# Kernel optimization log

Measured on AMD Instinct MI355X. Metric: run time of the kernel, lower is better.

Reference implementation:

```python
import jax, jax.numpy as jnp
import numpy as np

DIM = 512
NUM_HEADS = 8
HEAD_DIM = DIM // NUM_HEADS
LOCAL_HEADS = 4
WINDOW = 64
NEG_INF = -1e9


def setup_inputs() -> dict:
    key = jax.random.key(0)
    ks = jax.random.split(key, 5)
    B, N, C = 4, 8192, DIM
    x = jax.random.normal(ks[0], (B, N, C), dtype=jnp.float32)
    # nn.Linear weights stored as [out, in]; xavier-ish scale
    s = (2.0 / (C + C)) ** 0.5
    Wq = jax.random.normal(ks[1], (C, C), dtype=jnp.float32) * s
    Wkv = jax.random.normal(ks[2], (C, C), dtype=jnp.float32) * s
    Wproj = jax.random.normal(ks[3], (C, C), dtype=jnp.float32) * s
    bproj = jax.random.normal(ks[4], (C,), dtype=jnp.float32) * 0.01
    return {"x": x, "Wq": Wq, "Wkv": Wkv, "Wproj": Wproj, "bproj": bproj}


def _look_around(t):
    # t: [B,H,nw,m,d] -> [B,H,nw,3m,d] (prev window, current, next; zero-padded at ends)
    p = jnp.pad(t, ((0, 0), (0, 0), (1, 1), (0, 0), (0, 0)))
    return jnp.concatenate([p[:, :, :-2], p[:, :, 1:-1], p[:, :, 2:]], axis=3)


def _local_attn(q, k, v, m):
    # non-causal LocalAttention, look_backward=1, look_forward=1
    B, H, N, d = q.shape
    nw = N // m
    scale = d ** -0.5
    qw = q.reshape(B, H, nw, m, d)
    kw = _look_around(k.reshape(B, H, nw, m, d))
    vw = _look_around(v.reshape(B, H, nw, m, d))
    # mask out look-around positions that fall outside the sequence
    pos = jnp.arange(N).reshape(nw, m)
    pp = jnp.pad(pos, ((1, 1), (0, 0)), constant_values=-1)
    kpos = jnp.concatenate([pp[:-2], pp[1:-1], pp[2:]], axis=1)  # [nw, 3m]
    valid = (kpos >= 0)[None, None, :, None, :]
    scores = jnp.einsum('bhwid,bhwjd->bhwij', qw * scale, kw)
    scores = jnp.where(valid, scores, NEG_INF)
    attn = jax.nn.softmax(scores, axis=-1)
    out = jnp.einsum('bhwij,bhwjd->bhwid', attn, vw)
    return out.reshape(B, H, N, d)


def _linear_attn(q, k, v):
    d = q.shape[-1]
    q = jax.nn.softmax(q, axis=-1) * (d ** -0.5)
    k = jax.nn.softmax(k, axis=-2)
    context = jnp.einsum('bhnd,bhne->bhde', k, v)
    return jnp.einsum('bhnd,bhde->bhne', q, context)


def reference(x, Wq, Wkv, Wproj, bproj):
    B, N, C = x.shape
    m = WINDOW
    original_N = N
    rem = N % m  # static; 0 for chosen shapes
    if rem > 0:
        x = jnp.pad(x, ((0, 0), (m - rem, 0), (0, 0)))
        N = x.shape[1]
    q = x @ Wq.T
    k = x @ Wkv.T
    v = x @ Wkv.T  # source uses the same kv linear for both k and v
    merge = lambda t: t.reshape(B, N, -1, HEAD_DIM).transpose(0, 2, 1, 3)  # [B,H,N,d]
    q, k, v = merge(q), merge(k), merge(v)
    lh = LOCAL_HEADS
    lq, gq = q[:, :lh], q[:, lh:]
    lk, gk = k[:, :lh], k[:, lh:]
    lv, gv = v[:, :lh], v[:, lh:]
    outs = []
    if lh > 0:
        outs.append(_local_attn(lq, lk, lv, m))
    if q.shape[1] - lh > 0:
        outs.append(_linear_attn(gq, gk, gv))
    attn = jnp.concatenate(outs, axis=1)  # [B,H,N,d]
    y = attn.transpose(0, 2, 1, 3).reshape(B, N, -1)
    y = y[:, -original_N:]
    y = y @ Wproj.T + bproj
    return (y, attn)
```

## Files before the change

kernel.cpp:

```cpp
#include <hip/hip_runtime.h>

#define DIM 512
#define NH 8
#define HD 64
#define LH 4
#define WIN 64
#define BATCH 4
#define SEQ 8192
#define NWIN (SEQ/WIN)

typedef unsigned short u16;
typedef __bf16 bf16x8 __attribute__((ext_vector_type(8)));
typedef float f32x4 __attribute__((ext_vector_type(4)));

__device__ __forceinline__ float b2f(u16 u) {
    return __uint_as_float(((unsigned int)u) << 16);
}
__device__ __forceinline__ u16 f2b(float f) {
    unsigned int x = __float_as_uint(f);
    return (u16)((x + 0x7FFFu + ((x >> 16) & 1u)) >> 16);
}

__device__ __forceinline__ void gload16(const void* g, void* l) {
    __builtin_amdgcn_global_load_lds(
        (__attribute__((address_space(1))) void*)g,
        (__attribute__((address_space(3))) void*)l, 16, 0, 0);
}

__global__ void convert_bf16(const float* __restrict__ src, u16* __restrict__ dst, long n)
{
    long i = ((long)blockIdx.x * 256 + threadIdx.x) * 8;
    const long stride = (long)gridDim.x * 256 * 8;
    for (; i < n; i += stride) {
        uint4 a = *(const uint4*)(src + i), b = *(const uint4*)(src + i + 4);
        const float* af = (const float*)&a;
        const float* bf_ = (const float*)&b;
        uint4 o; u16* ou = (u16*)&o;
        #pragma unroll
        for (int j = 0; j < 4; j++) { ou[j] = f2b(af[j]); ou[4 + j] = f2b(bf_[j]); }
        *(uint4*)(dst + i) = o;
    }
}

__global__ void convert_w3(const float* __restrict__ Wq, const float* __restrict__ Wkv,
                           const float* __restrict__ Wp, u16* __restrict__ Wqk,
                           u16* __restrict__ Wproj_b)
{
    const int slice = blockIdx.y;
    const float* src = (slice == 0) ? Wq : (slice == 1) ? Wkv : Wp;
    u16* dst = (slice == 0) ? Wqk : (slice == 1) ? (Wqk + DIM * DIM) : Wproj_b;
    long i = ((long)blockIdx.x * 256 + threadIdx.x) * 8;
    if (i >= (long)DIM * DIM) return;
    uint4 a = *(const uint4*)(src + i), b = *(const uint4*)(src + i + 4);
    const float* af = (const float*)&a;
    const float* bf_ = (const float*)&b;
    uint4 o; u16* ou = (u16*)&o;
    #pragma unroll
    for (int j = 0; j < 4; j++) { ou[j] = f2b(af[j]); ou[4 + j] = f2b(bf_[j]); }
    *(uint4*)(dst + i) = o;
}

__global__ __launch_bounds__(256) void gemm_qk_tiled(const u16* __restrict__ xb,
        const u16* __restrict__ Wqk, u16* __restrict__ qh, u16* __restrict__ kh)
{
    __shared__ __align__(16) u16 smem[16384];
    u16* lA = smem;
    u16* lB = smem + 8192;

    const int tid = threadIdx.x;
    const int wv = tid >> 6, lane = tid & 63;
    const int quad = lane >> 4, l16 = lane & 15;
    const int wr = wv >> 1, wc = wv & 1;
    const int row0 = blockIdx.y * 128;
    const int col0 = blockIdx.x * 128;
    const int srow = lane >> 3;
    const int scol = ((lane & 7) ^ srow) * 8;

    f32x4 acc[4][4];
    #pragma unroll
    for (int t = 0; t < 4; t++)
        for (int u = 0; u < 4; u++)
            for (int i = 0; i < 4; i++) acc[t][u][i] = 0.f;

    const u16* gA = xb  + (size_t)(row0 + srow) * DIM + scol;
    const u16* gB = Wqk + (size_t)(col0 + srow) * DIM + scol;

    for (int kt = 0; kt < DIM; kt += 64) {
        __syncthreads();
        #pragma unroll
        for (int i = 0; i < 4; i++) {
            int rb = wv * 32 + i * 8;
            gload16(gA + (size_t)rb * DIM + kt, &lA[rb * 64]);
            gload16(gB + (size_t)rb * DIM + kt, &lB[rb * 64]);
        }
        __syncthreads();
        #pragma unroll
        for (int kc = 0; kc < 2; kc++) {
            bf16x8 af[4], bfr[4];
            #pragma unroll
            for (int t = 0; t < 4; t++) {
                int row = wr * 64 + t * 16 + l16;
                int slot = (kc * 4 + quad) ^ (row & 7);
                af[t] = *(const bf16x8*)&lA[row * 64 + slot * 8];
            }
            #pragma unroll
            for (int u = 0; u < 4; u++) {
                int row = wc * 64 + u * 16 + l16;
                int slot = (kc * 4 + quad) ^ (row & 7);
                bfr[u] = *(const bf16x8*)&lB[row * 64 + slot * 8];
            }
            #pragma unroll
            for (int t = 0; t < 4; t++)
                #pragma unroll
                for (int u = 0; u < 4; u++)
                    acc[t][u] = __builtin_amdgcn_mfma_f32_16x16x32_bf16(af[t], bfr[u], acc[t][u], 0, 0, 0);
        }
    }

    __syncthreads();
    u16* cw = smem + wv * 4096;
    #pragma unroll
    for (int t = 0; t < 4; t++)
        #pragma unroll
        for (int u = 0; u < 4; u++)
            #pragma unroll
            for (int r = 0; r < 4; r++)
                cw[(t * 16 + quad * 4 + r) * 64 + u * 16 + l16] = f2b(acc[t][u][r]);

    const int colg0 = col0 + wc * 64;
    const int seg = lane & 7;
    u16* dstbase;
    {
        int h = (colg0 & 511) >> 6;
        u16* base = (colg0 < 512) ? qh : kh;
        dstbase = base + (size_t)h * SEQ * HD;
    }
    #pragma unroll
    for (int i = 0; i < 8; i++) {
        int mm = i * 8 + (lane >> 3);
        uint4 v = *(const uint4*)&cw[mm * 64 + seg * 8];
        int m = row0 + wr * 64 + mm;
        int bb = m >> 13, nn = m & (SEQ - 1);
        *(uint4*)(dstbase + ((size_t)bb * NH * SEQ + nn) * HD + seg * 8) = v;
    }
}

#define KJ_STRIDE 72
#define KT_STRIDE 200
#define OT_STRIDE 80

__global__ __launch_bounds__(256) void local_attn(const u16* __restrict__ qh,
        const u16* __restrict__ kh, float* __restrict__ attn_out,
        u16* __restrict__ attn_b)
{
    __shared__ __align__(16) u16 kjP[192 * KJ_STRIDE];
    __shared__ __align__(16) u16 kT[64 * KT_STRIDE];

    const int w = blockIdx.x;
    const int bh = blockIdx.y;
    const int b = bh >> 2, h = bh & 3;
    const int tid = threadIdx.x;
    const int wv = tid >> 6, lane = tid & 63;
    const int quad = lane >> 4, l16 = lane & 15;

    for (int idx = tid; idx < 192 * 8; idx += 256) {
        int j = idx >> 3, dc = (idx & 7) << 3;
        int n = w * WIN - WIN + j;
        uint4 val = make_uint4(0, 0, 0, 0);
        if (n >= 0 && n < SEQ)
            val = *(const uint4*)(kh + (((size_t)(b * NH + h)) * SEQ + n) * HD + dc);
        *(uint4*)(&kjP[j * KJ_STRIDE + dc]) = val;
    }
    __syncthreads();
    for (int idx = tid; idx < 64 * 192; idx += 256) {
        int e = idx & 63, j = idx >> 6;
        kT[e * KT_STRIDE + j] = kjP[j * KJ_STRIDE + e];
    }
    __syncthreads();

    f32x4 s[12];
    #pragma unroll
    for (int t = 0; t < 12; t++)
        for (int i = 0; i < 4; i++) s[t][i] = 0.f;

    const u16* qrow = qh + (((size_t)(b * NH + h)) * SEQ + w * WIN + wv * 16 + l16) * HD + quad * 8;
    #pragma unroll
    for (int kk = 0; kk < 64; kk += 32) {
        bf16x8 a = *(const bf16x8*)(qrow + kk);
        #pragma unroll
        for (int t = 0; t < 12; t++) {
            bf16x8 bf = *(const bf16x8*)(&kjP[(t * 16 + l16) * KJ_STRIDE + kk + quad * 8]);
            s[t] = __builtin_amdgcn_mfma_f32_16x16x32_bf16(a, bf, s[t], 0, 0, 0);
        }
    }
    __syncthreads();

    const float scale = 0.125f;
    #pragma unroll
    for (int r = 0; r < 4; r++) {
        float vals[12];
        float mx = -3.0e38f;
        #pragma unroll
        for (int t = 0; t < 12; t++) {
            int j = t * 16 + l16;
            float v = s[t][r] * scale;
            bool valid = !((w == 0 && j < 64) || (w == NWIN - 1 && j >= 128));
            v = valid ? v : -30000.0f;
            vals[t] = v;
            mx = fmaxf(mx, v);
        }
        for (int m = 1; m <= 8; m <<= 1) mx = fmaxf(mx, __shfl_xor(mx, m));
        float sum = 0.f;
        #pragma unroll
        for (int t = 0; t < 12; t++) { vals[t] = __expf(vals[t] - mx); sum += vals[t]; }
        for (int m = 1; m <= 8; m <<= 1) sum += __shfl_xor(sum, m);
        float inv = 1.0f / sum;
        int prow = wv * 16 + quad * 4 + r;
        #pragma unroll
        for (int t = 0; t < 12; t++)
            kjP[prow * KT_STRIDE + t * 16 + l16] = f2b(vals[t] * inv);
    }
    __syncthreads();

    f32x4 o[4];
    #pragma unroll
    for (int t = 0; t < 4; t++)
        for (int i = 0; i < 4; i++) o[t][i] = 0.f;
    #pragma unroll
    for (int kc = 0; kc < 6; kc++) {
        bf16x8 a = *(const bf16x8*)(&kjP[(wv * 16 + l16) * KT_STRIDE + kc * 32 + quad * 8]);
        #pragma unroll
        for (int t = 0; t < 4; t++) {
            bf16x8 bf = *(const bf16x8*)(&kT[(t * 16 + l16) * KT_STRIDE + kc * 32 + quad * 8]);
            o[t] = __builtin_amdgcn_mfma_f32_16x16x32_bf16(a, bf, o[t], 0, 0, 0);
        }
    }
    #pragma unroll
    for (int t = 0; t < 4; t++) {
        int e = t * 16 + l16;
        #pragma unroll
        for (int r = 0; r < 4; r++) {
            int n = w * WIN + wv * 16 + quad * 4 + r;
            attn_out[(((size_t)(b * NH + h)) * SEQ + n) * HD + e] = o[t][r];
        }
    }
    __syncthreads();
    #pragma unroll
    for (int t = 0; t < 4; t++)
        #pragma unroll
        for (int r = 0; r < 4; r++)
            kT[(wv * 16 + quad * 4 + r) * OT_STRIDE + t * 16 + l16] = f2b(o[t][r]);
    __syncthreads();
    for (int idx = tid; idx < 512; idx += 256) {
        int row = idx >> 3, seg = (idx & 7) * 8;
        uint4 v = *(const uint4*)&kT[row * OT_STRIDE + seg];
        *(uint4*)(attn_b + ((size_t)(b * SEQ + w * WIN + row)) * DIM + h * HD + seg) = v;
    }
}

__global__ __launch_bounds__(256) void ctx_accum(const u16* __restrict__ kh,
        float* __restrict__ partials, float* __restrict__ colsum)
{
    const int chunk = blockIdx.x;
    const int bh = blockIdx.y;
    const int b = bh >> 2, hg = bh & 3;
    const int tid = threadIdx.x;
    const int wv = tid >> 6, lane = tid & 63;
    const int d0 = (lane >> 2) * 4;
    const int e0 = (lane & 3) * 16;

    __shared__ __align__(16) float smem[2 * 64 * 68];
    float* kraw = smem;
    float* kexp = smem + 64 * 68;

    f32x4 acc[4][4];
    #pragma unroll
    for (int dd = 0; dd < 4; dd++)
        #pragma unroll
        for (int j = 0; j < 4; j++)
            for (int i = 0; i < 4; i++) acc[dd][j][i] = 0.f;
    f32x4 csum;
    for (int i = 0; i < 4; i++) csum[i] = 0.f;

    const u16* kbase = kh + ((size_t)(b * NH + LH + hg)) * SEQ * HD
                          + (size_t)chunk * 256 * HD;

    for (int ph = 0; ph < 4; ph++) {
        __syncthreads();
        #pragma unroll
        for (int pass = 0; pass < 2; pass++) {
            int idx = pass * 256 + tid;
            int row = idx >> 3, seg = (idx & 7) * 8;
            uint4 v = *(const uint4*)(kbase + ((size_t)(ph * 64 + row)) * HD + seg);
            const u16* u = (const u16*)&v;
            f32x4 r0, r1, E0, E1;
            #pragma unroll
            for (int j = 0; j < 4; j++) {
                r0[j] = b2f(u[j]);      E0[j] = __expf(r0[j]);
                r1[j] = b2f(u[4 + j]);  E1[j] = __expf(r1[j]);
            }
            float* kr = &kraw[row * 68 + seg];
            float* ke = &kexp[row * 68 + seg];
            *(f32x4*)kr = r0;  *(f32x4*)(kr + 4) = r1;
            *(f32x4*)ke = E0;  *(f32x4*)(ke + 4) = E1;
        }
        __syncthreads();
        #pragma unroll 4
        for (int i = 0; i < 16; i++) {
            int roff = (wv * 16 + i) * 68;
            f32x4 ek = *(const f32x4*)&kexp[roff + d0];
            const f32x4* kv = (const f32x4*)&kraw[roff + e0];
            f32x4 k0 = kv[0], k1 = kv[1], k2 = kv[2], k3 = kv[3];
            csum += ek;
            #pragma unroll
            for (int dd = 0; dd < 4; dd++) {
                acc[dd][0] += ek[dd] * k0;
                acc[dd][1] += ek[dd] * k1;
                acc[dd][2] += ek[dd] * k2;
                acc[dd][3] += ek[dd] * k3;
            }
        }
    }

    float* red0 = smem;
    float* red1 = smem + 4160;
    __syncthreads();
    if (wv >= 2) {
        float* rd = (wv == 2) ? red0 : red1;
        #pragma unroll
        for (int dd = 0; dd < 4; dd++)
            #pragma unroll
            for (int j = 0; j < 4; j++)
                *(f32x4*)&rd[(d0 + dd) * 64 + e0 + j * 4] = acc[dd][j];
        if ((lane & 3) == 0) *(f32x4*)&rd[4096 + d0] = csum;
    }
    __syncthreads();
    if (wv < 2) {
        float* rd = (wv == 0) ? red0 : red1;
        #pragma unroll
        for (int dd = 0; dd < 4; dd++)
            #pragma unroll
            for (int j = 0; j < 4; j++)
                acc[dd][j] += *(const f32x4*)&rd[(d0 + dd) * 64 + e0 + j * 4];
        csum += *(const f32x4*)&rd[4096 + d0];
    }
    __syncthreads();
    if (wv == 1) {
        #pragma unroll
        for (int dd = 0; dd < 4; dd++)
            #pragma unroll
            for (int j = 0; j < 4; j++)
                *(f32x4*)&red0[(d0 + dd) * 64 + e0 + j * 4] = acc[dd][j];
        if ((lane & 3) == 0) *(f32x4*)&red0[4096 + d0] = csum;
    }
    __syncthreads();
    if (wv == 0) {
        float* P = partials + ((size_t)(chunk * 16 + bh)) * 4096;
        #pragma unroll
        for (int dd = 0; dd < 4; dd++)
            #pragma unroll
            for (int j = 0; j < 4; j++) {
                f32x4 r = acc[dd][j] + *(const f32x4*)&red0[(d0 + dd) * 64 + e0 + j * 4];
                *(f32x4*)&P[(d0 + dd) * 64 + e0 + j * 4] = r;
            }
        if ((lane & 3) == 0) {
            f32x4 cs = csum + *(const f32x4*)&red0[4096 + d0];
            #pragma unroll
            for (int dd = 0; dd < 4; dd++)
                atomicAdd(colsum + bh * 64 + d0 + dd, cs[dd]);
        }
    }
}

__global__ __launch_bounds__(256) void reduce_ctx(const float* __restrict__ partials,
        const float* __restrict__ colsum, u16* __restrict__ ctxT)
{
    const int quarter = blockIdx.x;
    const int bh = blockIdx.y;
    const int tid = threadIdx.x;
    __shared__ float cs[64];
    if (tid < 64) cs[tid] = colsum[bh * 64 + tid];
    __syncthreads();
    const int i0 = quarter * 1024;
    for (int idx = i0 + tid; idx < i0 + 1024; idx += 256) {
        float s = 0.f;
        #pragma unroll 8
        for (int c = 0; c < 32; c++)
            s += partials[((size_t)(c * 16 + bh)) * 4096 + idx];
        int d = idx >> 6, e = idx & 63;
        ctxT[(size_t)bh * 4096 + e * 64 + d] = f2b(s / cs[d]);
    }
}

__global__ __launch_bounds__(256) void global_out(const u16* __restrict__ qh,
        const u16* __restrict__ ctxT, float* __restrict__ attn_out,
        u16* __restrict__ attn_b)
{
    const int nblk = blockIdx.x;
    const int bh = blockIdx.y;
    const int b = bh >> 2, hg = bh & 3;
    const int tid = threadIdx.x;
    const int wv = tid >> 6, lane = tid & 63;
    const int quad = lane >> 4, l16 = lane & 15;

    __shared__ __align__(16) u16 ctxL[64 * 64];
    __shared__ __align__(16) u16 ot[64 * OT_STRIDE];

    {
        const int srow = lane >> 3;
        const int scol = ((lane & 7) ^ srow) * 8;
        const u16* src = ctxT + (size_t)bh * 4096 + (size_t)srow * 64 + scol;
        #pragma unroll
        for (int j = 0; j < 2; j++) {
            int rb = j * 32 + wv * 8;
            gload16(src + rb * 64, &ctxL[rb * 64]);
        }
    }

    const int n0 = nblk * 64;
    const u16* qp = qh + (((size_t)(b * NH + LH + hg)) * SEQ + n0 + wv * 16 + l16) * HD + quad * 8;
    uint4 v0 = *(const uint4*)(qp);
    uint4 v1 = *(const uint4*)(qp + 32);
    const u16* u0 = (const u16*)&v0;
    const u16* u1 = (const u16*)&v1;
    float e0[8], e1[8];
    float s = 0.f;
    #pragma unroll
    for (int j = 0; j < 8; j++) { e0[j] = __expf(b2f(u0[j])); s += e0[j]; }
    #pragma unroll
    for (int j = 0; j < 8; j++) { e1[j] = __expf(b2f(u1[j])); s += e1[j]; }
    s += __shfl_xor(s, 16);
    s += __shfl_xor(s, 32);
    const float inv = 0.125f / s;
    uint4 p0u, p1u;
    u16* p0 = (u16*)&p0u; u16* p1 = (u16*)&p1u;
    #pragma unroll
    for (int j = 0; j < 8; j++) { p0[j] = f2b(e0[j] * inv); p1[j] = f2b(e1[j] * inv); }
    bf16x8 pa0 = *(const bf16x8*)&p0u;
    bf16x8 pa1 = *(const bf16x8*)&p1u;

    __syncthreads();

    f32x4 acc[4];
    #pragma unroll
    for (int u = 0; u < 4; u++)
        for (int i = 0; i < 4; i++) acc[u][i] = 0.f;
    #pragma unroll
    for (int u = 0; u < 4; u++) {
        int row = u * 16 + l16;
        int s0 = (0 + quad) ^ (row & 7);
        int s1 = (4 + quad) ^ (row & 7);
        bf16x8 b0 = *(const bf16x8*)&ctxL[row * 64 + s0 * 8];
        bf16x8 b1 = *(const bf16x8*)&ctxL[row * 64 + s1 * 8];
        acc[u] = __builtin_amdgcn_mfma_f32_16x16x32_bf16(pa0, b0, acc[u], 0, 0, 0);
        acc[u] = __builtin_amdgcn_mfma_f32_16x16x32_bf16(pa1, b1, acc[u], 0, 0, 0);
    }

    const size_t obase = ((size_t)(b * NH + LH + hg)) * SEQ + n0 + wv * 16;
    #pragma unroll
    for (int u = 0; u < 4; u++) {
        int ee = u * 16 + l16;
        #pragma unroll
        for (int r = 0; r < 4; r++)
            attn_out[(obase + quad * 4 + r) * HD + ee] = acc[u][r];
    }

    #pragma unroll
    for (int u = 0; u < 4; u++)
        #pragma unroll
        for (int r = 0; r < 4; r++)
            ot[(wv * 16 + quad * 4 + r) * OT_STRIDE + u * 16 + l16] = f2b(acc[u][r]);
    __syncthreads();
    for (int idx = tid; idx < 512; idx += 256) {
        int row = idx >> 3, seg = (idx & 7) * 8;
        uint4 vv = *(const uint4*)&ot[row * OT_STRIDE + seg];
        *(uint4*)(attn_b + ((size_t)(b * SEQ + n0 + row)) * DIM + (LH + hg) * HD + seg) = vv;
    }
}

__global__ __launch_bounds__(256) void proj_gemm_tiled(const u16* __restrict__ attn_b,
        const u16* __restrict__ Wproj, const float* __restrict__ bproj,
        float* __restrict__ y)
{
    __shared__ __align__(16) u16 smem[16384];
    u16* lA = smem;
    u16* lB = smem + 8192;

    const int tid = threadIdx.x;
    const int wv = tid >> 6, lane = tid & 63;
    const int quad = lane >> 4, l16 = lane & 15;
    const int wr = wv >> 1, wc = wv & 1;
    const int row0 = blockIdx.y * 128;
    const int col0 = blockIdx.x * 128;
    const int srow = lane >> 3;
    const int scol = ((lane & 7) ^ srow) * 8;

    f32x4 acc[4][4];
    #pragma unroll
    for (int t = 0; t < 4; t++)
        for (int u = 0; u < 4; u++)
            for (int i = 0; i < 4; i++) acc[t][u][i] = 0.f;

    const u16* gA = attn_b + (size_t)(row0 + srow) * DIM + scol;
    const u16* gB = Wproj  + (size_t)(col0 + srow) * DIM + scol;

    for (int kt = 0; kt < DIM; kt += 64) {
        __syncthreads();
        #pragma unroll
        for (int i = 0; i < 4; i++) {
            int rb = wv * 32 + i * 8;
            gload16(gA + (size_t)rb * DIM + kt, &lA[rb * 64]);
            gload16(gB + (size_t)rb * DIM + kt, &lB[rb * 64]);
        }
        __syncthreads();
        #pragma unroll
        for (int kc = 0; kc < 2; kc++) {
            bf16x8 af[4], bfr[4];
            #pragma unroll
            for (int t = 0; t < 4; t++) {
                int row = wr * 64 + t * 16 + l16;
                int slot = (kc * 4 + quad) ^ (row & 7);
                af[t] = *(const bf16x8*)&lA[row * 64 + slot * 8];
            }
            #pragma unroll
            for (int u = 0; u < 4; u++) {
                int row = wc * 64 + u * 16 + l16;
                int slot = (kc * 4 + quad) ^ (row & 7);
                bfr[u] = *(const bf16x8*)&lB[row * 64 + slot * 8];
            }
            #pragma unroll
            for (int t = 0; t < 4; t++)
                #pragma unroll
                for (int u = 0; u < 4; u++)
                    acc[t][u] = __builtin_amdgcn_mfma_f32_16x16x32_bf16(af[t], bfr[u], acc[t][u], 0, 0, 0);
        }
    }

    #pragma unroll
    for (int u = 0; u < 4; u++) {
        int col = col0 + wc * 64 + u * 16 + l16;
        float bias = bproj[col];
        #pragma unroll
        for (int t = 0; t < 4; t++)
            #pragma unroll
            for (int r = 0; r < 4; r++) {
                int m = row0 + wr * 64 + t * 16 + quad * 4 + r;
                y[(size_t)m * DIM + col] = acc[t][u][r] + bias;
            }
    }
}

extern "C" void kernel_launch(void* const* d_in, const int* in_sizes, int n_in,
                              void* d_out, int out_size, void* d_ws, size_t ws_size,
                              hipStream_t stream)
{
    (void)in_sizes; (void)n_in; (void)out_size; (void)ws_size;
    const float* x     = (const float*)d_in[0];
    const float* Wq    = (const float*)d_in[1];
    const float* Wkv   = (const float*)d_in[2];
    const float* Wproj = (const float*)d_in[3];
    const float* bproj = (const float*)d_in[4];

    float* y        = (float*)d_out;
    float* attn_out = y + (size_t)BATCH * SEQ * DIM;

    u16* xb = (u16*)y;
    u16* qh = xb + (size_t)BATCH * SEQ * DIM;

    float* partials = attn_out + (size_t)LH * SEQ * HD;

    char* ws = (char*)d_ws;
    u16*   ctxT    = (u16*)ws;
    float* colsum  = (float*)(ws + 262144);
    u16*   Wqk     = (u16*)(ws + 266240);
    u16*   Wproj_b = (u16*)(ws + 266240 + 1048576);
    u16*   kh      = (u16*)(ws + 266240 + 1048576 + 524288);
    u16*   attn_b  = kh + (size_t)BATCH * SEQ * DIM;

    const long NX = (long)BATCH * SEQ * DIM;

    hipMemsetAsync(colsum, 0, 4096, stream);
    convert_bf16<<<4096, 256, 0, stream>>>(x, xb, NX);
    convert_w3<<<dim3(128, 3), 256, 0, stream>>>(Wq, Wkv, Wproj, Wqk, Wproj_b);

    gemm_qk_tiled<<<dim3(8, 256), 256, 0, stream>>>(xb, Wqk, qh, kh);
    local_attn<<<dim3(NWIN, 16), 256, 0, stream>>>(qh, kh, attn_out, attn_b);
    ctx_accum<<<dim3(32, 16), 256, 0, stream>>>(kh, partials, colsum);
    reduce_ctx<<<dim3(4, 16), 256, 0, stream>>>(partials, colsum, ctxT);
    global_out<<<dim3(SEQ / 64, 16), 256, 0, stream>>>(qh, ctxT, attn_out, attn_b);
    proj_gemm_tiled<<<dim3(4, 256), 256, 0, stream>>>(attn_b, Wproj_b, bproj, y);
}
```

Before: 345.2 us.

## Compute linear-attention context with MFMA using transposed K written by QK GEMM

The QK GEMM now also writes a transposed copy of the global-head K ([b,h,d,n]) into workspace. ctx_accum reads that transposed layout, computes exp(K) in bf16, and forms exp(K)^T K with bf16 MFMA instead of scalar fp32 FMAs. This drops the cross-wave LDS reduction and the fp32 staging. The trade-off is extra global writes in the GEMM epilogue and bf16 rounding of exp(K) in both the context and the column sums.

Result: no change. 341.1 us (-1.2%).

```diff
diff --git a/kernel.cpp b/kernel.cpp
--- a/kernel.cpp
+++ b/kernel.cpp
@@ -61,7 +61,8 @@
 }
 
 __global__ __launch_bounds__(256) void gemm_qk_tiled(const u16* __restrict__ xb,
-        const u16* __restrict__ Wqk, u16* __restrict__ qh, u16* __restrict__ kh)
+        const u16* __restrict__ Wqk, u16* __restrict__ qh, u16* __restrict__ kh,
+        u16* __restrict__ khTg)
 {
     __shared__ __align__(16) u16 smem[16384];
     u16* lA = smem;
@@ -143,6 +144,22 @@
         int bb = m >> 13, nn = m & (SEQ - 1);
         *(uint4*)(dstbase + ((size_t)bb * NH * SEQ + nn) * HD + seg * 8) = v;
     }
+
+    if (colg0 >= 768) {
+        int hg = ((colg0 & 511) >> 6) - 4;
+        int m0 = row0 + wr * 64;
+        int bb = m0 >> 13, nn0 = m0 & (SEQ - 1);
+        u16* kT = khTg + ((size_t)((bb << 2) + hg) * 64) * SEQ + nn0;
+        #pragma unroll
+        for (int i = 0; i < 8; i++) {
+            int e = i * 8 + (lane >> 3);
+            int ns = (lane & 7) * 8;
+            uint4 ov; u16* op = (u16*)&ov;
+            #pragma unroll
+            for (int j = 0; j < 8; j++) op[j] = cw[(ns + j) * 64 + e];
+            *(uint4*)(kT + (size_t)e * SEQ + ns) = ov;
+        }
+    }
 }
 
 #define KJ_STRIDE 72
@@ -258,118 +275,82 @@
     }
 }
 
-__global__ __launch_bounds__(256) void ctx_accum(const u16* __restrict__ kh,
+__global__ __launch_bounds__(256) void ctx_accum(const u16* __restrict__ khTg,
         float* __restrict__ partials, float* __restrict__ colsum)
 {
     const int chunk = blockIdx.x;
     const int bh = blockIdx.y;
-    const int b = bh >> 2, hg = bh & 3;
     const int tid = threadIdx.x;
     const int wv = tid >> 6, lane = tid & 63;
-    const int d0 = (lane >> 2) * 4;
-    const int e0 = (lane & 3) * 16;
-
-    __shared__ __align__(16) float smem[2 * 64 * 68];
-    float* kraw = smem;
-    float* kexp = smem + 64 * 68;
-
-    f32x4 acc[4][4];
-    #pragma unroll
-    for (int dd = 0; dd < 4; dd++)
-        #pragma unroll
-        for (int j = 0; j < 4; j++)
-            for (int i = 0; i < 4; i++) acc[dd][j][i] = 0.f;
-    f32x4 csum;
-    for (int i = 0; i < 4; i++) csum[i] = 0.f;
-
-    const u16* kbase = kh + ((size_t)(b * NH + LH + hg)) * SEQ * HD
-                          + (size_t)chunk * 256 * HD;
-
-    for (int ph = 0; ph < 4; ph++) {
+    const int quad = lane >> 4, l16 = lane & 15;
+
+    __shared__ __align__(16) u16 rawL[64 * 64];
+    __shared__ __align__(16) u16 expL[64 * 64];
+
+    const u16* base = khTg + (size_t)bh * 64 * SEQ;
+    const int dexp = tid >> 2;
+    const int nsub = (tid & 3) * 16;
+
+    const int srow = lane >> 3;
+    const int scol = ((lane & 7) ^ srow) * 8;
+
+    f32x4 acc[4];
+    #pragma unroll
+    for (int u = 0; u < 4; u++)
+        for (int i = 0; i < 4; i++) acc[u][i] = 0.f;
+    float csum = 0.f;
+
+    for (int t = 0; t < 4; t++) {
+        const int n0 = chunk * 256 + t * 64;
         __syncthreads();
         #pragma unroll
-        for (int pass = 0; pass < 2; pass++) {
-            int idx = pass * 256 + tid;
-            int row = idx >> 3, seg = (idx & 7) * 8;
-            uint4 v = *(const uint4*)(kbase + ((size_t)(ph * 64 + row)) * HD + seg);
-            const u16* u = (const u16*)&v;
-            f32x4 r0, r1, E0, E1;
-            #pragma unroll
-            for (int j = 0; j < 4; j++) {
-                r0[j] = b2f(u[j]);      E0[j] = __expf(r0[j]);
-                r1[j] = b2f(u[4 + j]);  E1[j] = __expf(r1[j]);
-            }
-            float* kr = &kraw[row * 68 + seg];
-            float* ke = &kexp[row * 68 + seg];
-            *(f32x4*)kr = r0;  *(f32x4*)(kr + 4) = r1;
-            *(f32x4*)ke = E0;  *(f32x4*)(ke + 4) = E1;
+        for (int i = 0; i < 2; i++) {
+            int r0 = wv * 16 + i * 8;
+            gload16(base + (size_t)(r0 + srow) * SEQ + n0 + scol, &rawL[r0 * 64]);
+        }
+        {
+            const u16* g = base + (size_t)dexp * SEQ + n0 + nsub;
+            uint4 v0 = *(const uint4*)g;
+            uint4 v1 = *(const uint4*)(g + 8);
+            const u16* ua = (const u16*)&v0;
+            const u16* ub = (const u16*)&v1;
+            uint4 o0, o1; u16* pa = (u16*)&o0; u16* pb = (u16*)&o1;
+            #pragma unroll
+            for (int j = 0; j < 8; j++) {
+                u16 ra = f2b(__expf(b2f(ua[j])));
+                u16 rb = f2b(__expf(b2f(ub[j])));
+                pa[j] = ra; pb[j] = rb;
+                csum += b2f(ra) + b2f(rb);
+            }
+            int sl0 = ((nsub >> 3) + 0) ^ (dexp & 7);
+            int sl1 = ((nsub >> 3) + 1) ^ (dexp & 7);
+            *(uint4*)&expL[dexp * 64 + sl0 * 8] = o0;
+            *(uint4*)&expL[dexp * 64 + sl1 * 8] = o1;
         }
         __syncthreads();
-        #pragma unroll 4
-        for (int i = 0; i < 16; i++) {
-            int roff = (wv * 16 + i) * 68;
-            f32x4 ek = *(const f32x4*)&kexp[roff + d0];
-            const f32x4* kv = (const f32x4*)&kraw[roff + e0];
-            f32x4 k0 = kv[0], k1 = kv[1], k2 = kv[2], k3 = kv[3];
-            csum += ek;
-            #pragma unroll
-            for (int dd = 0; dd < 4; dd++) {
-                acc[dd][0] += ek[dd] * k0;
-                acc[dd][1] += ek[dd] * k1;
-                acc[dd][2] += ek[dd] * k2;
-                acc[dd][3] += ek[dd] * k3;
-            }
-        }
-    }
-
-    float* red0 = smem;
-    float* red1 = smem + 4160;
-    __syncthreads();
-    if (wv >= 2) {
-        float* rd = (wv == 2) ? red0 : red1;
-        #pragma unroll
-        for (int dd = 0; dd < 4; dd++)
-            #pragma unroll
-            for (int j = 0; j < 4; j++)
-                *(f32x4*)&rd[(d0 + dd) * 64 + e0 + j * 4] = acc[dd][j];
-        if ((lane & 3) == 0) *(f32x4*)&rd[4096 + d0] = csum;
-    }
-    __syncthreads();
-    if (wv < 2) {
-        float* rd = (wv == 0) ? red0 : red1;
-        #pragma unroll
-        for (int dd = 0; dd < 4; dd++)
-            #pragma unroll
-            for (int j = 0; j < 4; j++)
-                acc[dd][j] += *(const f32x4*)&rd[(d0 + dd) * 64 + e0 + j * 4];
-        csum += *(const f32x4*)&rd[4096 + d0];
-    }
-    __syncthreads();
-    if (wv == 1) {
-        #pragma unroll
-        for (int dd = 0; dd < 4; dd++)
-            #pragma unroll
-            for (int j = 0; j < 4; j++)
-                *(f32x4*)&red0[(d0 + dd) * 64 + e0 + j * 4] = acc[dd][j];
-        if ((lane & 3) == 0) *(f32x4*)&red0[4096 + d0] = csum;
-    }
-    __syncthreads();
-    if (wv == 0) {
-        float* P = partials + ((size_t)(chunk * 16 + bh)) * 4096;
-        #pragma unroll
-        for (int dd = 0; dd < 4; dd++)
-            #pragma unroll
-            for (int j = 0; j < 4; j++) {
-                f32x4 r = acc[dd][j] + *(const f32x4*)&red0[(d0 + dd) * 64 + e0 + j * 4];
-                *(f32x4*)&P[(d0 + dd) * 64 + e0 + j * 4] = r;
-            }
-        if ((lane & 3) == 0) {
-            f32x4 cs = csum + *(const f32x4*)&red0[4096 + d0];
-            #pragma unroll
-            for (int dd = 0; dd < 4; dd++)
-                atomicAdd(colsum + bh * 64 + d0 + dd, cs[dd]);
-        }
-    }
+        #pragma unroll
+        for (int kc = 0; kc < 2; kc++) {
+            int arow = wv * 16 + l16;
+            bf16x8 af = *(const bf16x8*)&expL[arow * 64 + (((kc * 4 + quad) ^ (arow & 7)) * 8)];
+            #pragma unroll
+            for (int u = 0; u < 4; u++) {
+                int brow = u * 16 + l16;
+                bf16x8 bf = *(const bf16x8*)&rawL[brow * 64 + (((kc * 4 + quad) ^ (brow & 7)) * 8)];
+                acc[u] = __builtin_amdgcn_mfma_f32_16x16x32_bf16(af, bf, acc[u], 0, 0, 0);
+            }
+        }
+    }
+
+    float* P = partials + ((size_t)(chunk * 16 + bh)) * 4096;
+    #pragma unroll
+    for (int u = 0; u < 4; u++)
+        #pragma unroll
+        for (int r = 0; r < 4; r++)
+            P[(wv * 16 + quad * 4 + r) * 64 + u * 16 + l16] = acc[u][r];
+
+    csum += __shfl_xor(csum, 1);
+    csum += __shfl_xor(csum, 2);
+    if ((tid & 3) == 0) atomicAdd(colsum + bh * 64 + dexp, csum);
 }
 
 __global__ __launch_bounds__(256) void reduce_ctx(const float* __restrict__ partials,
@@ -576,6 +557,7 @@
     u16*   Wproj_b = (u16*)(ws + 266240 + 1048576);
     u16*   kh      = (u16*)(ws + 266240 + 1048576 + 524288);
     u16*   attn_b  = kh + (size_t)BATCH * SEQ * DIM;
+    u16*   khTg    = attn_b + (size_t)BATCH * SEQ * DIM;
 
     const long NX = (long)BATCH * SEQ * DIM;
 
@@ -583,9 +565,9 @@
     convert_bf16<<<4096, 256, 0, stream>>>(x, xb, NX);
     convert_w3<<<dim3(128, 3), 256, 0, stream>>>(Wq, Wkv, Wproj, Wqk, Wproj_b);
 
-    gemm_qk_tiled<<<dim3(8, 256), 256, 0, stream>>>(xb, Wqk, qh, kh);
+    gemm_qk_tiled<<<dim3(8, 256), 256, 0, stream>>>(xb, Wqk, qh, kh, khTg);
     local_attn<<<dim3(NWIN, 16), 256, 0, stream>>>(qh, kh, attn_out, attn_b);
-    ctx_accum<<<dim3(32, 16), 256, 0, stream>>>(kh, partials, colsum);
+    ctx_accum<<<dim3(32, 16), 256, 0, stream>>>(khTg, partials, colsum);
     reduce_ctx<<<dim3(4, 16), 256, 0, stream>>>(partials, colsum, ctxT);
     global_out<<<dim3(SEQ / 64, 16), 256, 0, stream>>>(qh, ctxT, attn_out, attn_b);
     proj_gemm_tiled<<<dim3(4, 256), 256, 0, stream>>>(attn_b, Wproj_b, bproj, y);
```
